# Kernel tuning notes

Measured on AMD Instinct MI355X. Metric: run time of the kernel, lower is better.

The kernel has to match this reference:

```python
import jax, jax.numpy as jnp
import numpy as np

N0, N1, N2 = 100000, 150000, 80000
E = 1000000
D_IN, D_OUT = 128, 128


def setup_inputs() -> dict:
    key = jax.random.key(0)
    ks = jax.random.split(key, 20)
    s_in = 1.0 / np.sqrt(D_IN)
    s_out = 1.0 / np.sqrt(D_OUT)
    s_agg = 1.0 / np.sqrt(4 * D_OUT)
    return {
        "x0": jax.random.normal(ks[0], (N0, D_IN), jnp.float32),
        "x1": jax.random.normal(ks[1], (N1, D_IN), jnp.float32),
        "x2": jax.random.normal(ks[2], (N2, D_IN), jnp.float32),
        # Linearlayer1: torch Linear(input_size, output_size); stored as (D_IN, D_OUT) => y = x @ W1 + b1
        "W1": jax.random.uniform(ks[3], (D_IN, D_OUT), jnp.float32, -s_in, s_in),
        "b1": jax.random.uniform(ks[4], (D_OUT,), jnp.float32, -s_in, s_in),
        # a_1, a_2: Linear(output_size, 1) -> weight vector (D_OUT,), scalar bias
        "a1_w": jax.random.uniform(ks[5], (D_OUT,), jnp.float32, -s_out, s_out),
        "a1_b": jax.random.uniform(ks[6], (), jnp.float32, -s_out, s_out),
        "a2_w": jax.random.uniform(ks[7], (D_OUT,), jnp.float32, -s_out, s_out),
        "a2_b": jax.random.uniform(ks[8], (), jnp.float32, -s_out, s_out),
        # LinearAgg: Linear(4*output_size, output_size)
        "Wagg": jax.random.uniform(ks[9], (4 * D_OUT, D_OUT), jnp.float32, -s_agg, s_agg),
        "bagg": jax.random.uniform(ks[10], (D_OUT,), jnp.float32, -s_agg, s_agg),
        # sparse incidence matrices as COO edge lists (rows index into n0)
        "adj0_rows": jax.random.randint(ks[11], (E,), 0, N0, jnp.int32),
        "adj0_cols": jax.random.randint(ks[12], (E,), 0, N0, jnp.int32),
        "adj1_rows": jax.random.randint(ks[13], (E,), 0, N0, jnp.int32),
        "adj1_cols": jax.random.randint(ks[14], (E,), 0, N1, jnp.int32),
        "adj2_rows": jax.random.randint(ks[15], (E,), 0, N0, jnp.int32),
        "adj2_cols": jax.random.randint(ks[16], (E,), 0, N2, jnp.int32),
    }


def _attention_agg(xi, xj, rows, cols, a1_w, a1_b, a2_w, a2_b, n_out):
    # edge-wise attention score: sigmoid(a1(xi)[row] + a2(xj)[col]); never build the dense n x n matrix
    a1 = xi @ a1_w + a1_b  # (n_i,)
    a2 = xj @ a2_w + a2_b  # (n_j,)
    att = jax.nn.sigmoid(a1[rows] + a2[cols])  # (E,)
    # sparse.mm(attention, xj): scatter-add att_e * xj[col_e] into row_e
    return jax.ops.segment_sum(att[:, None] * xj[cols], rows, num_segments=n_out)


def reference(x0, x1, x2, W1, b1, a1_w, a1_b, a2_w, a2_b, Wagg, bagg,
              adj0_rows, adj0_cols, adj1_rows, adj1_cols, adj2_rows, adj2_cols):
    lin1 = lambda x: jax.nn.relu(x @ W1 + b1)
    xi_0 = lin1(x0)  # xi_0 == xj_0 in the original (same layer, same input)
    xj_1 = lin1(x1)
    xj_2 = lin1(x2)
    n0 = x0.shape[0]
    agg0 = _attention_agg(xi_0, xi_0, adj0_rows, adj0_cols, a1_w, a1_b, a2_w, a2_b, n0)
    agg1 = _attention_agg(xi_0, xj_1, adj1_rows, adj1_cols, a1_w, a1_b, a2_w, a2_b, n0)
    agg2 = _attention_agg(xi_0, xj_2, adj2_rows, adj2_cols, a1_w, a1_b, a2_w, a2_b, n0)
    cat = jnp.concatenate([xi_0, agg0, agg1, agg2], axis=1)  # (n0, 4*D_OUT)
    return cat @ Wagg + bagg
```

## Files before the change

### kernel.cpp

```cpp
#include <hip/hip_runtime.h>

typedef unsigned int uint32;
typedef unsigned short ushort16;

constexpr int CN0 = 100000;
constexpr int CN1 = 150000;
constexpr int CN2 = 80000;
constexpr int CNE = 1000000;
constexpr int CD  = 128;
constexpr int NBINS = 3 * CN0;
constexpr int TOT_E = 3 * CNE;

constexpr int NB    = (NBINS + 511) / 512;
constexpr int CHUNK = 8192;
constexpr int G     = (TOT_E + CHUNK - 1) / CHUNK;
constexpr int NBG   = NB * G;
constexpr int CSCAN_BLOCKS = (NBG + 1023) / 1024;

constexpr size_t align256(size_t x) { return (x + 255) & ~(size_t)255; }

constexpr size_t OFF_H0B = 0;
constexpr size_t OFF_H1B = align256(OFF_H0B + (size_t)CN0 * CD * 2);
constexpr size_t OFF_H2B = align256(OFF_H1B + (size_t)CN1 * CD * 2);
constexpr size_t OFF_AG1 = align256(OFF_H2B + (size_t)CN2 * CD * 2);
constexpr size_t OFF_AG2 = align256(OFF_AG1 + (size_t)CN0 * CD * 2);
constexpr size_t OFF_A1  = align256(OFF_AG2 + (size_t)CN0 * CD * 2);
constexpr size_t OFF_A2  = align256(OFF_A1 + (size_t)CN0 * 4);
constexpr size_t OFF_RS  = align256(OFF_A2 + (size_t)(CN0 + CN1 + CN2) * 4);
constexpr size_t OFF_BH  = align256(OFF_RS + (size_t)(NBINS + 1) * 4);
constexpr size_t OFF_SCL = align256(OFF_BH + (size_t)NBG * 4);
constexpr size_t OFF_BS  = align256(OFF_SCL + (size_t)TOT_E * 4);
constexpr size_t OFF_BB  = align256(OFF_BS + (size_t)CSCAN_BLOCKS * 4);
constexpr size_t OFF_END = OFF_BB + (size_t)CN0 * CD * 2;

__device__ inline float b2f(ushort16 u) {
  union { uint32 i; float f; } v; v.i = ((uint32)u) << 16; return v.f;
}
__device__ inline ushort16 f2b(float f) {
  union { float f; uint32 i; } v; v.f = f;
  uint32 r = (v.i + 0x7FFFu + ((v.i >> 16) & 1u)) >> 16;
  return (ushort16)r;
}
__device__ inline uint32 pack2(float a, float b) {
  return (uint32)f2b(a) | ((uint32)f2b(b) << 16);
}
__device__ inline float2 load2(const ushort16* p, size_t i) {
  uint32 u = *(const uint32*)(p + i);
  union { uint32 i; float f; } lo, hi;
  lo.i = u << 16; hi.i = u & 0xFFFF0000u;
  return make_float2(lo.f, hi.f);
}

typedef __bf16 bf16x8 __attribute__((ext_vector_type(8)));
typedef float f32x4 __attribute__((ext_vector_type(4)));
union FragU { uint4 q; bf16x8 v; ushort16 u[8]; };

template <int NP, bool RELU, bool DOT1, bool DOT2, typename TA, typename TC>
__global__ __launch_bounds__(256) void gemm_mfma(
    const TA* __restrict__ A0, const TA* __restrict__ A1,
    const TA* __restrict__ A2, const TA* __restrict__ A3,
    const float* __restrict__ W, const float* __restrict__ bias,
    TC* __restrict__ C, int M,
    const float* __restrict__ a1w, const float* __restrict__ a2w,
    const float* __restrict__ a1b, const float* __restrict__ a2b,
    float* __restrict__ dot1out, float* __restrict__ dot2out) {
  constexpr int WS = 136;
  __shared__ ushort16 Wt[128 * WS];

  const int t = threadIdx.x;
  const int wave = t >> 6;
  const int lane = t & 63;
  const int ln = lane & 15;
  const int quad = lane >> 4;
  const int row0 = blockIdx.x * 64;
  const int rowA = row0 + wave * 16 + ln;
  const int rA = (rowA < M) ? rowA : (M - 1);
  const int rowC = row0 + wave * 16 + quad * 4;

  f32x4 acc[8];
#pragma unroll
  for (int j = 0; j < 8; ++j) acc[j] = (f32x4)(0.f);

#pragma unroll
  for (int p = 0; p < NP; ++p) {
    const TA* __restrict__ Ap = (p == 0) ? A0 : ((p == 1) ? A1 : ((p == 2) ? A2 : A3));
    const float* __restrict__ Wp = W + (size_t)p * CD * CD;
    if (p > 0) __syncthreads();
    for (int i = t; i < CD * CD; i += 256) {
      int k = i >> 7, n = i & 127;
      Wt[n * WS + k] = f2b(Wp[i]);
    }
    __syncthreads();
#pragma unroll
    for (int ks = 0; ks < 4; ++ks) {
      const int k0 = ks * 32;
      FragU af;
      if constexpr (sizeof(TA) == 2) {
        af.q = *(const uint4*)((const ushort16*)Ap + (size_t)rA * CD + k0 + quad * 8);
      } else {
        const float* ap = (const float*)Ap + (size_t)rA * CD + k0 + quad * 8;
        float4 f0 = *(const float4*)ap;
        float4 f1 = *(const float4*)(ap + 4);
        af.u[0] = f2b(f0.x); af.u[1] = f2b(f0.y); af.u[2] = f2b(f0.z); af.u[3] = f2b(f0.w);
        af.u[4] = f2b(f1.x); af.u[5] = f2b(f1.y); af.u[6] = f2b(f1.z); af.u[7] = f2b(f1.w);
      }
#pragma unroll
      for (int j = 0; j < 8; ++j) {
        FragU bf;
        bf.q = *(const uint4*)&Wt[(j * 16 + ln) * WS + k0 + quad * 8];
        acc[j] = __builtin_amdgcn_mfma_f32_16x16x32_bf16(af.v, bf.v, acc[j], 0, 0, 0);
      }
    }
  }

  float s1[4] = {0.f, 0.f, 0.f, 0.f};
  float s2[4] = {0.f, 0.f, 0.f, 0.f};
#pragma unroll
  for (int j = 0; j < 8; ++j) {
    const int n = j * 16 + ln;
    const float bj = bias[n];
    const float a1wj = DOT1 ? a1w[n] : 0.f;
    const float a2wj = DOT2 ? a2w[n] : 0.f;
#pragma unroll
    for (int r = 0; r < 4; ++r) {
      float v = acc[j][r] + bj;
      if constexpr (RELU) v = fmaxf(v, 0.f);
      const int row = rowC + r;
      if (row < M) {
        if constexpr (sizeof(TC) == 2)
          ((ushort16*)C)[(size_t)row * CD + n] = f2b(v);
        else
          ((float*)C)[(size_t)row * CD + n] = v;
      }
      if constexpr (DOT1) s1[r] = fmaf(v, a1wj, s1[r]);
      if constexpr (DOT2) s2[r] = fmaf(v, a2wj, s2[r]);
    }
  }
  if constexpr (DOT1 || DOT2) {
#pragma unroll
    for (int mask = 1; mask < 16; mask <<= 1) {
#pragma unroll
      for (int r = 0; r < 4; ++r) {
        if constexpr (DOT1) s1[r] += __shfl_xor(s1[r], mask);
        if constexpr (DOT2) s2[r] += __shfl_xor(s2[r], mask);
      }
    }
    if (ln == 0) {
#pragma unroll
      for (int r = 0; r < 4; ++r) {
        const int row = rowC + r;
        if (row < M) {
          if constexpr (DOT2) dot2out[row] = s2[r] + a2b[0];
          if constexpr (DOT1) dot1out[row] = s1[r] + a1b[0];
        }
      }
    }
  }
}

__device__ inline int edge_bin(int e, const int* r0, const int* r1, const int* r2) {
  if (e < CNE) return r0[e];
  if (e < 2 * CNE) return CN0 + r1[e - CNE];
  return 2 * CN0 + r2[e - 2 * CNE];
}
__device__ inline void edge_get(int e, const int* r0, const int* c0, const int* r1,
                                const int* c1, const int* r2, const int* c2,
                                int& bin, int& col) {
  if (e < CNE) { bin = r0[e]; col = c0[e]; }
  else if (e < 2 * CNE) { bin = CN0 + r1[e - CNE]; col = c1[e - CNE]; }
  else { bin = 2 * CN0 + r2[e - 2 * CNE]; col = c2[e - 2 * CNE]; }
}

__global__ __launch_bounds__(256) void coarse_hist_kernel(
    const int* __restrict__ r0, const int* __restrict__ r1, const int* __restrict__ r2,
    int* __restrict__ blockhist) {
  __shared__ int lh[NB];
  const int t = threadIdx.x;
  for (int i = t; i < NB; i += 256) lh[i] = 0;
  __syncthreads();
  const int e0 = blockIdx.x * CHUNK;
  for (int i = t; i < CHUNK; i += 256) {
    int e = e0 + i;
    if (e < TOT_E) atomicAdd(&lh[edge_bin(e, r0, r1, r2) >> 9], 1);
  }
  __syncthreads();
  for (int i = t; i < NB; i += 256) blockhist[(size_t)i * G + blockIdx.x] = lh[i];
}

__global__ void scan1g_kernel(int* __restrict__ data, int* __restrict__ bsums, int n) {
  __shared__ int lds[256];
  int t = threadIdx.x;
  int idx0 = blockIdx.x * 1024 + t * 4;
  int v[4];
#pragma unroll
  for (int j = 0; j < 4; ++j) v[j] = (idx0 + j < n) ? data[idx0 + j] : 0;
  int tsum = v[0] + v[1] + v[2] + v[3];
  lds[t] = tsum;
  __syncthreads();
  for (int off = 1; off < 256; off <<= 1) {
    int x = (t >= off) ? lds[t - off] : 0;
    __syncthreads();
    lds[t] += x;
    __syncthreads();
  }
  int run = lds[t] - tsum;
  if (t == 255) bsums[blockIdx.x] = lds[255];
#pragma unroll
  for (int j = 0; j < 4; ++j) {
    if (idx0 + j < n) data[idx0 + j] = run;
    run += v[j];
  }
}

__global__ void scan2g_kernel(int* __restrict__ bsums, int nb) {
  __shared__ int lds[512];
  int t = threadIdx.x;
  int v = (t < nb) ? bsums[t] : 0;
  lds[t] = v;
  __syncthreads();
  for (int off = 1; off < 512; off <<= 1) {
    int x = (t >= off) ? lds[t - off] : 0;
    __syncthreads();
    lds[t] += x;
    __syncthreads();
  }
  if (t < nb) bsums[t] = lds[t] - v;
}

__global__ void scan3g_kernel(int* __restrict__ data, const int* __restrict__ bsums, int n) {
  int t = threadIdx.x;
  int idx0 = blockIdx.x * 1024 + t * 4;
  int off = bsums[blockIdx.x];
#pragma unroll
  for (int j = 0; j < 4; ++j)
    if (idx0 + j < n) data[idx0 + j] += off;
}

__global__ __launch_bounds__(256) void reorder_kernel(
    const int* __restrict__ r0, const int* __restrict__ c0,
    const int* __restrict__ r1, const int* __restrict__ c1,
    const int* __restrict__ r2, const int* __restrict__ c2,
    const int* __restrict__ blockscan, uint32* __restrict__ bbuf) {
  __shared__ int lbase[NB];
  const int t = threadIdx.x;
  for (int i = t; i < NB; i += 256) lbase[i] = blockscan[(size_t)i * G + blockIdx.x];
  __syncthreads();
  const int e0 = blockIdx.x * CHUNK;
  for (int i = t; i < CHUNK; i += 256) {
    int e = e0 + i;
    if (e >= TOT_E) break;
    int bin, col;
    edge_get(e, r0, c0, r1, c1, r2, c2, bin, col);
    int pos = atomicAdd(&lbase[bin >> 9], 1);
    bbuf[pos] = ((uint32)(bin & 511) << 18) | (uint32)col;
  }
}

__global__ __launch_bounds__(256) void finalize_kernel(
    const int* __restrict__ blockscan, const uint32* __restrict__ bbuf,
    const float* __restrict__ a1_0, const float* __restrict__ a2all,
    uint32* __restrict__ scols, int* __restrict__ rs) {
  __shared__ int lh[512];
  __shared__ int sc[256];
  const int t = threadIdx.x;
  const int b = blockIdx.x;
  const int binbase = b << 9;
  const int gs = blockscan[(size_t)b * G];
  const int ge = (b == NB - 1) ? TOT_E : blockscan[(size_t)(b + 1) * G];
  const int cnt = ge - gs;

  lh[2 * t] = 0;
  lh[2 * t + 1] = 0;
  __syncthreads();
  for (int i = t; i < cnt; i += 256) atomicAdd(&lh[bbuf[gs + i] >> 18], 1);
  __syncthreads();
  int v0 = lh[2 * t], v1 = lh[2 * t + 1];
  int tsum = v0 + v1;
  sc[t] = tsum;
  __syncthreads();
  for (int off = 1; off < 256; off <<= 1) {
    int x = (t >= off) ? sc[t - off] : 0;
    __syncthreads();
    sc[t] += x;
    __syncthreads();
  }
  int ex = sc[t] - tsum;
  lh[2 * t] = ex;
  lh[2 * t + 1] = ex + v0;
  int nb_here = NBINS - binbase;
  if (2 * t < nb_here) rs[binbase + 2 * t] = gs + ex;
  if (2 * t + 1 < nb_here) rs[binbase + 2 * t + 1] = gs + ex + v0;
  if (b == NB - 1 && t == 255) rs[NBINS] = TOT_E;
  __syncthreads();
  for (int i = t; i < cnt; i += 256) {
    uint32 p = bbuf[gs + i];
    int bl = (int)(p >> 18);
    int col = (int)(p & 0x3FFFFu);
    int gbin = binbase + bl;
    int a = (gbin >= 2 * CN0) ? 2 : ((gbin >= CN0) ? 1 : 0);
    int row = gbin - a * CN0;
    int aoff = (a == 0) ? 0 : ((a == 1) ? CN0 : CN0 + CN1);
    float z = a1_0[row] + a2all[aoff + col];
    float att = 1.0f / (1.0f + __expf(-z));
    int q = (int)(att * 16384.f);
    if (q > 16383) q = 16383;
    int pos = atomicAdd(&lh[bl], 1);
    scols[gs + pos] = ((uint32)q << 18) | (uint32)col;
  }
}

__global__ void agg_kernel_all(const int* __restrict__ rs, const uint32* __restrict__ scols,
                               const ushort16* __restrict__ h0,
                               const ushort16* __restrict__ h1,
                               const ushort16* __restrict__ h2,
                               ushort16* __restrict__ agg0, ushort16* __restrict__ agg1,
                               ushort16* __restrict__ agg2) {
  int w = (blockIdx.x * blockDim.x + threadIdx.x) >> 6;
  if (w >= NBINS) return;
  int lane = threadIdx.x & 63;
  int a = (w >= 2 * CN0) ? 2 : ((w >= CN0) ? 1 : 0);
  const ushort16* __restrict__ xj = (a == 0) ? h0 : ((a == 1) ? h1 : h2);
  ushort16* __restrict__ out = (a == 0) ? agg0 : ((a == 1) ? agg1 : agg2);
  int row = w - a * CN0;
  int s = rs[w], e = rs[w + 1];
  float ax = 0.f, ay = 0.f;
  const size_t loff = (size_t)lane * 2;
  int p = s;
  constexpr float SC = 1.0f / 16384.f;
  for (; p + 4 <= e; p += 4) {
    uint32 k0 = scols[p], k1 = scols[p + 1], k2 = scols[p + 2], k3 = scols[p + 3];
    float2 v0 = load2(xj, (size_t)(k0 & 0x3FFFFu) * CD + loff);
    float2 v1 = load2(xj, (size_t)(k1 & 0x3FFFFu) * CD + loff);
    float2 v2 = load2(xj, (size_t)(k2 & 0x3FFFFu) * CD + loff);
    float2 v3 = load2(xj, (size_t)(k3 & 0x3FFFFu) * CD + loff);
    float t0 = ((float)(k0 >> 18) + 0.5f) * SC;
    float t1 = ((float)(k1 >> 18) + 0.5f) * SC;
    float t2 = ((float)(k2 >> 18) + 0.5f) * SC;
    float t3 = ((float)(k3 >> 18) + 0.5f) * SC;
    ax = fmaf(t0, v0.x, ax); ay = fmaf(t0, v0.y, ay);
    ax = fmaf(t1, v1.x, ax); ay = fmaf(t1, v1.y, ay);
    ax = fmaf(t2, v2.x, ax); ay = fmaf(t2, v2.y, ay);
    ax = fmaf(t3, v3.x, ax); ay = fmaf(t3, v3.y, ay);
  }
  for (; p < e; ++p) {
    uint32 k = scols[p];
    float2 v = load2(xj, (size_t)(k & 0x3FFFFu) * CD + loff);
    float tt = ((float)(k >> 18) + 0.5f) * SC;
    ax = fmaf(tt, v.x, ax); ay = fmaf(tt, v.y, ay);
  }
  *(uint32*)(out + (size_t)row * CD + loff) = pack2(ax, ay);
}

extern "C" void kernel_launch(void* const* d_in, const int* in_sizes, int n_in,
                              void* d_out, int out_size, void* d_ws, size_t ws_size,
                              hipStream_t stream) {
  const float* x0 = (const float*)d_in[0];
  const float* x1 = (const float*)d_in[1];
  const float* x2 = (const float*)d_in[2];
  const float* W1 = (const float*)d_in[3];
  const float* b1 = (const float*)d_in[4];
  const float* a1_w = (const float*)d_in[5];
  const float* a1_b = (const float*)d_in[6];
  const float* a2_w = (const float*)d_in[7];
  const float* a2_b = (const float*)d_in[8];
  const float* Wagg = (const float*)d_in[9];
  const float* bagg = (const float*)d_in[10];
  const int* adj0_r = (const int*)d_in[11];
  const int* adj0_c = (const int*)d_in[12];
  const int* adj1_r = (const int*)d_in[13];
  const int* adj1_c = (const int*)d_in[14];
  const int* adj2_r = (const int*)d_in[15];
  const int* adj2_c = (const int*)d_in[16];
  float* out = (float*)d_out;

  if (ws_size < OFF_END) return;

  char* ws = (char*)d_ws;
  ushort16* h0b    = (ushort16*)(ws + OFF_H0B);
  ushort16* h1b    = (ushort16*)(ws + OFF_H1B);
  ushort16* h2b    = (ushort16*)(ws + OFF_H2B);
  ushort16* agg1b  = (ushort16*)(ws + OFF_AG1);
  ushort16* agg2b  = (ushort16*)(ws + OFF_AG2);
  float*    a1_0   = (float*)(ws + OFF_A1);
  float*    a2all  = (float*)(ws + OFF_A2);
  int*      rs     = (int*)(ws + OFF_RS);
  int*      bh     = (int*)(ws + OFF_BH);
  uint32*   scols  = (uint32*)(ws + OFF_SCL);
  int*      bsums  = (int*)(ws + OFF_BS);
  uint32*   bbuf   = (uint32*)(ws + OFF_BB);
  ushort16* agg0b  = (ushort16*)(ws + OFF_BB);

  gemm_mfma<1, true, true, true, float, ushort16><<<(CN0 + 63) / 64, 256, 0, stream>>>(
      x0, x0, x0, x0, W1, b1, h0b, CN0, a1_w, a2_w, a1_b, a2_b, a1_0, a2all);
  gemm_mfma<1, true, false, true, float, ushort16><<<(CN1 + 63) / 64, 256, 0, stream>>>(
      x1, x1, x1, x1, W1, b1, h1b, CN1, a1_w, a2_w, a1_b, a2_b, a1_0, a2all + CN0);
  gemm_mfma<1, true, false, true, float, ushort16><<<(CN2 + 63) / 64, 256, 0, stream>>>(
      x2, x2, x2, x2, W1, b1, h2b, CN2, a1_w, a2_w, a1_b, a2_b, a1_0, a2all + CN0 + CN1);

  coarse_hist_kernel<<<G, 256, 0, stream>>>(adj0_r, adj1_r, adj2_r, bh);
  scan1g_kernel<<<CSCAN_BLOCKS, 256, 0, stream>>>(bh, bsums, NBG);
  scan2g_kernel<<<1, 512, 0, stream>>>(bsums, CSCAN_BLOCKS);
  scan3g_kernel<<<CSCAN_BLOCKS, 256, 0, stream>>>(bh, bsums, NBG);
  reorder_kernel<<<G, 256, 0, stream>>>(adj0_r, adj0_c, adj1_r, adj1_c,
                                        adj2_r, adj2_c, bh, bbuf);
  finalize_kernel<<<NB, 256, 0, stream>>>(bh, bbuf, a1_0, a2all, scols, rs);

  agg_kernel_all<<<(NBINS * 64 + 255) / 256, 256, 0, stream>>>(
      rs, scols, h0b, h1b, h2b, agg0b, agg1b, agg2b);

  gemm_mfma<4, false, false, false, ushort16, float><<<(CN0 + 63) / 64, 256, 0, stream>>>(
      h0b, agg0b, agg1b, agg2b, Wagg, bagg, out, CN0,
      a1_w, a2_w, a1_b, a2_b, nullptr, nullptr);
}
```

Measured before the change: 591.0 us.

## Switch intermediates to fp16 and pack four rows per wave in aggregation

Intermediate features, GEMM operands and the MFMA instruction move from bf16 to fp16, which keeps more mantissa at the same storage size. The aggregation kernel now assigns 16 lanes per output row, four rows per wave, and each lane loads 16 bytes (eight halves) per edge instead of 4 bytes. Loop trip count is the maximum edge count among the four rows, with masked tail edges. This cuts the number of wave-level instructions per gathered row and raises the width of each memory request. The trade-off is divergence waste when degrees differ within a wave, and fp16 overflow risk on large activations.

```diff
diff --git a/kernel.cpp b/kernel.cpp
--- a/kernel.cpp
+++ b/kernel.cpp
@@ -33,27 +33,21 @@
 constexpr size_t OFF_BB  = align256(OFF_BS + (size_t)CSCAN_BLOCKS * 4);
 constexpr size_t OFF_END = OFF_BB + (size_t)CN0 * CD * 2;
 
-__device__ inline float b2f(ushort16 u) {
-  union { uint32 i; float f; } v; v.i = ((uint32)u) << 16; return v.f;
-}
-__device__ inline ushort16 f2b(float f) {
-  union { float f; uint32 i; } v; v.f = f;
-  uint32 r = (v.i + 0x7FFFu + ((v.i >> 16) & 1u)) >> 16;
-  return (ushort16)r;
-}
-__device__ inline uint32 pack2(float a, float b) {
-  return (uint32)f2b(a) | ((uint32)f2b(b) << 16);
-}
-__device__ inline float2 load2(const ushort16* p, size_t i) {
-  uint32 u = *(const uint32*)(p + i);
-  union { uint32 i; float f; } lo, hi;
-  lo.i = u << 16; hi.i = u & 0xFFFF0000u;
-  return make_float2(lo.f, hi.f);
-}
-
-typedef __bf16 bf16x8 __attribute__((ext_vector_type(8)));
+typedef _Float16 f16x2 __attribute__((ext_vector_type(2)));
+typedef _Float16 f16x8 __attribute__((ext_vector_type(8)));
+typedef __fp16 fp16x2_builtin __attribute__((ext_vector_type(2)));
+
+__device__ inline ushort16 f2h(float f) {
+  union { _Float16 h; ushort16 u; } v; v.h = (_Float16)f; return v.u;
+}
+__device__ inline uint32 packh2(float a, float b) {
+  union { fp16x2_builtin h; uint32 u; } v;
+  v.h = __builtin_amdgcn_cvt_pkrtz(a, b);
+  return v.u;
+}
+
 typedef float f32x4 __attribute__((ext_vector_type(4)));
-union FragU { uint4 q; bf16x8 v; ushort16 u[8]; };
+union FragU { uint4 q; f16x8 v; ushort16 u[8]; };
 
 template <int NP, bool RELU, bool DOT1, bool DOT2, typename TA, typename TC>
 __global__ __launch_bounds__(256) void gemm_mfma(
@@ -88,7 +82,7 @@
     if (p > 0) __syncthreads();
     for (int i = t; i < CD * CD; i += 256) {
       int k = i >> 7, n = i & 127;
-      Wt[n * WS + k] = f2b(Wp[i]);
+      Wt[n * WS + k] = f2h(Wp[i]);
     }
     __syncthreads();
 #pragma unroll
@@ -101,14 +95,14 @@
         const float* ap = (const float*)Ap + (size_t)rA * CD + k0 + quad * 8;
         float4 f0 = *(const float4*)ap;
         float4 f1 = *(const float4*)(ap + 4);
-        af.u[0] = f2b(f0.x); af.u[1] = f2b(f0.y); af.u[2] = f2b(f0.z); af.u[3] = f2b(f0.w);
-        af.u[4] = f2b(f1.x); af.u[5] = f2b(f1.y); af.u[6] = f2b(f1.z); af.u[7] = f2b(f1.w);
+        af.u[0] = f2h(f0.x); af.u[1] = f2h(f0.y); af.u[2] = f2h(f0.z); af.u[3] = f2h(f0.w);
+        af.u[4] = f2h(f1.x); af.u[5] = f2h(f1.y); af.u[6] = f2h(f1.z); af.u[7] = f2h(f1.w);
       }
 #pragma unroll
       for (int j = 0; j < 8; ++j) {
         FragU bf;
         bf.q = *(const uint4*)&Wt[(j * 16 + ln) * WS + k0 + quad * 8];
-        acc[j] = __builtin_amdgcn_mfma_f32_16x16x32_bf16(af.v, bf.v, acc[j], 0, 0, 0);
+        acc[j] = __builtin_amdgcn_mfma_f32_16x16x32_f16(af.v, bf.v, acc[j], 0, 0, 0);
       }
     }
   }
@@ -128,7 +122,7 @@
       const int row = rowC + r;
       if (row < M) {
         if constexpr (sizeof(TC) == 2)
-          ((ushort16*)C)[(size_t)row * CD + n] = f2b(v);
+          ((ushort16*)C)[(size_t)row * CD + n] = f2h(v);
         else
           ((float*)C)[(size_t)row * CD + n] = v;
       }
@@ -309,46 +303,73 @@
   }
 }
 
-__global__ void agg_kernel_all(const int* __restrict__ rs, const uint32* __restrict__ scols,
-                               const ushort16* __restrict__ h0,
-                               const ushort16* __restrict__ h1,
-                               const ushort16* __restrict__ h2,
-                               ushort16* __restrict__ agg0, ushort16* __restrict__ agg1,
-                               ushort16* __restrict__ agg2) {
-  int w = (blockIdx.x * blockDim.x + threadIdx.x) >> 6;
-  if (w >= NBINS) return;
-  int lane = threadIdx.x & 63;
-  int a = (w >= 2 * CN0) ? 2 : ((w >= CN0) ? 1 : 0);
-  const ushort16* __restrict__ xj = (a == 0) ? h0 : ((a == 1) ? h1 : h2);
-  ushort16* __restrict__ out = (a == 0) ? agg0 : ((a == 1) ? agg1 : agg2);
-  int row = w - a * CN0;
-  int s = rs[w], e = rs[w + 1];
-  float ax = 0.f, ay = 0.f;
-  const size_t loff = (size_t)lane * 2;
+__global__ __launch_bounds__(256) void agg_kernel_all(
+    const int* __restrict__ rs, const uint32* __restrict__ scols,
+    const ushort16* __restrict__ h0,
+    const ushort16* __restrict__ h1,
+    const ushort16* __restrict__ h2,
+    ushort16* __restrict__ agg0, ushort16* __restrict__ agg1,
+    ushort16* __restrict__ agg2) {
+  const int waveid = (blockIdx.x * blockDim.x + threadIdx.x) >> 6;
+  const int g = (threadIdx.x >> 4) & 3;
+  const int ln = threadIdx.x & 15;
+  const uint32 eoff = (uint32)ln << 4;
+
+  const int w = waveid * 4 + g;
+  const bool active = (w < NBINS);
+  const int wc = active ? w : (NBINS - 1);
+
+  const int a = (wc >= 2 * CN0) ? 2 : ((wc >= CN0) ? 1 : 0);
+  const char* __restrict__ xj =
+      (const char*)((a == 0) ? h0 : ((a == 1) ? h1 : h2));
+  char* __restrict__ outp = (char*)((a == 0) ? agg0 : ((a == 1) ? agg1 : agg2));
+  const int row = wc - a * CN0;
+
+  int s = rs[wc], e = rs[wc + 1];
+  if (!active) { s = 0; e = 0; }
+  const int pc0 = (e > s) ? (e - 1) : 0;
+
+  constexpr float SC = 1.0f / 16384.f;
+  float acc[8];
+#pragma unroll
+  for (int j = 0; j < 8; ++j) acc[j] = 0.f;
+
+  int mm = e - s;
+  mm = max(mm, __shfl_xor(mm, 16));
+  mm = max(mm, __shfl_xor(mm, 32));
+
   int p = s;
-  constexpr float SC = 1.0f / 16384.f;
-  for (; p + 4 <= e; p += 4) {
-    uint32 k0 = scols[p], k1 = scols[p + 1], k2 = scols[p + 2], k3 = scols[p + 3];
-    float2 v0 = load2(xj, (size_t)(k0 & 0x3FFFFu) * CD + loff);
-    float2 v1 = load2(xj, (size_t)(k1 & 0x3FFFFu) * CD + loff);
-    float2 v2 = load2(xj, (size_t)(k2 & 0x3FFFFu) * CD + loff);
-    float2 v3 = load2(xj, (size_t)(k3 & 0x3FFFFu) * CD + loff);
-    float t0 = ((float)(k0 >> 18) + 0.5f) * SC;
-    float t1 = ((float)(k1 >> 18) + 0.5f) * SC;
-    float t2 = ((float)(k2 >> 18) + 0.5f) * SC;
-    float t3 = ((float)(k3 >> 18) + 0.5f) * SC;
-    ax = fmaf(t0, v0.x, ax); ay = fmaf(t0, v0.y, ay);
-    ax = fmaf(t1, v1.x, ax); ay = fmaf(t1, v1.y, ay);
-    ax = fmaf(t2, v2.x, ax); ay = fmaf(t2, v2.y, ay);
-    ax = fmaf(t3, v3.x, ax); ay = fmaf(t3, v3.y, ay);
-  }
-  for (; p < e; ++p) {
-    uint32 k = scols[p];
-    float2 v = load2(xj, (size_t)(k & 0x3FFFFu) * CD + loff);
-    float tt = ((float)(k >> 18) + 0.5f) * SC;
-    ax = fmaf(tt, v.x, ax); ay = fmaf(tt, v.y, ay);
-  }
-  *(uint32*)(out + (size_t)row * CD + loff) = pack2(ax, ay);
+  auto round = [&](int q) {
+    const int pc = (q < e) ? q : pc0;
+    const uint32 k = scols[pc];
+    const uint4 v = *(const uint4*)(xj + (((k & 0x3FFFFu) << 8) | eoff));
+    const float tv = fmaf((float)(k >> 18), SC, 0.5f * SC);
+    const float t = (q < e) ? tv : 0.f;
+    union { uint4 q4; f16x2 h[4]; } u;
+    u.q4 = v;
+    acc[0] = fmaf((float)u.h[0][0], t, acc[0]);
+    acc[1] = fmaf((float)u.h[0][1], t, acc[1]);
+    acc[2] = fmaf((float)u.h[1][0], t, acc[2]);
+    acc[3] = fmaf((float)u.h[1][1], t, acc[3]);
+    acc[4] = fmaf((float)u.h[2][0], t, acc[4]);
+    acc[5] = fmaf((float)u.h[2][1], t, acc[5]);
+    acc[6] = fmaf((float)u.h[3][0], t, acc[6]);
+    acc[7] = fmaf((float)u.h[3][1], t, acc[7]);
+  };
+  for (int i = 0; i < mm; i += 2) {
+    round(p);
+    round(p + 1);
+    p += 2;
+  }
+
+  if (active) {
+    uint4 o;
+    o.x = packh2(acc[0], acc[1]);
+    o.y = packh2(acc[2], acc[3]);
+    o.z = packh2(acc[4], acc[5]);
+    o.w = packh2(acc[6], acc[7]);
+    *(uint4*)(outp + (((size_t)row << 8) | eoff)) = o;
+  }
 }
 
 extern "C" void kernel_launch(void* const* d_in, const int* in_sizes, int n_in,
@@ -405,8 +426,12 @@
                                         adj2_r, adj2_c, bh, bbuf);
   finalize_kernel<<<NB, 256, 0, stream>>>(bh, bbuf, a1_0, a2all, scols, rs);
 
-  agg_kernel_all<<<(NBINS * 64 + 255) / 256, 256, 0, stream>>>(
-      rs, scols, h0b, h1b, h2b, agg0b, agg1b, agg2b);
+  {
+    const int nwaves = (NBINS + 3) / 4;
+    const int nblocks = (nwaves * 64 + 255) / 256;
+    agg_kernel_all<<<nblocks, 256, 0, stream>>>(
+        rs, scols, h0b, h1b, h2b, agg0b, agg1b, agg2b);
+  }
 
   gemm_mfma<4, false, false, false, ushort16, float><<<(CN0 + 63) / 64, 256, 0, stream>>>(
       h0b, agg0b, agg1b, agg2b, Wagg, bagg, out, CN0,
```

New measurement: 551.1 us. 6.7% less time.
